# Kernel tuning notes

Measured on AMD Instinct MI355X. Metric: run time of the kernel, lower is better.

The kernel has to match this reference:

```python
import jax, jax.numpy as jnp
import numpy as np

N_NODES = 100000
N_EDGES = 1600000
NODE_DIM = 64
EDGE_DIM = 16
HIDDEN = 64
N_LAYERS = 3
N_GRAPHS = 512
BN_EPS = 1e-5


def setup_inputs() -> dict:
    key = jax.random.key(0)
    ks = jax.random.split(key, 12)
    x = jax.random.normal(ks[0], (N_NODES, NODE_DIM), dtype=jnp.float32)
    edge_index = jax.random.randint(ks[1], (2, N_EDGES), 0, N_NODES, dtype=jnp.int32)
    edge_attr = jax.random.normal(ks[2], (N_EDGES, EDGE_DIM), dtype=jnp.float32)
    batch = jnp.sort(jax.random.randint(ks[3], (N_NODES,), 0, N_GRAPHS, dtype=jnp.int32))
    s = 0.1
    # stacked per-layer params (node_dim == hidden so all layers share shapes)
    We = jax.random.normal(ks[4], (N_LAYERS, EDGE_DIM, HIDDEN), dtype=jnp.float32) * s
    be = jnp.zeros((N_LAYERS, HIDDEN), dtype=jnp.float32)
    W1 = jax.random.normal(ks[5], (N_LAYERS, HIDDEN, HIDDEN), dtype=jnp.float32) * s
    b1 = jnp.zeros((N_LAYERS, HIDDEN), dtype=jnp.float32)
    W2 = jax.random.normal(ks[6], (N_LAYERS, HIDDEN, HIDDEN), dtype=jnp.float32) * s
    b2 = jnp.zeros((N_LAYERS, HIDDEN), dtype=jnp.float32)
    gamma = jnp.ones((N_LAYERS, HIDDEN), dtype=jnp.float32)
    beta = jnp.zeros((N_LAYERS, HIDDEN), dtype=jnp.float32)
    return {"x": x, "edge_attr": edge_attr, "We": We, "be": be, "W1": W1,
            "b1": b1, "W2": W2, "b2": b2, "gamma": gamma, "beta": beta,
            "edge_index": edge_index, "batch": batch}


def reference(x, edge_attr, We, be, W1, b1, W2, b2, gamma, beta, edge_index, batch):
    src, dst = edge_index[0], edge_index[1]
    n_nodes = x.shape[0]
    z = x
    zs = []
    for l in range(We.shape[0]):
        # GINEConv: message = relu(x_j + Lin(edge_attr)); aggr = scatter_add at dst
        e = edge_attr @ We[l] + be[l]                       # [E, H]
        msg = jax.nn.relu(z[src] + e)                       # [E, H]
        aggr = jax.ops.segment_sum(msg, dst, num_segments=n_nodes)  # [N, H]
        h = z + aggr                                        # (1 + eps)*x, eps=0
        h = jax.nn.relu(h @ W1[l] + b1[l]) @ W2[l] + b2[l]  # GINE nn MLP
        h = jax.nn.relu(h)
        # BatchNorm1d in training mode: biased batch stats over nodes
        mean = jnp.mean(h, axis=0)
        var = jnp.mean(jnp.square(h - mean), axis=0)
        h = gamma[l] * (h - mean) * jax.lax.rsqrt(var + BN_EPS) + beta[l]
        z = h
        zs.append(h)
    zz = jnp.concatenate(zs, axis=1)                        # [N, L*H]
    g = jax.ops.segment_sum(zz, batch, num_segments=N_GRAPHS)  # [G, L*H]
    return zz, g
```

## Files before the change

kernel.cpp:

```cpp
#include <hip/hip_runtime.h>

#define N_NODES 100000
#define N_EDGES 1600000
#define HIDDEN 64
#define EDGE_DIM 16
#define N_LAYERS 3
#define N_GRAPHS 512
#define BN_EPS 1e-5f

#define CHUNK 2048
#define NCHUNK ((N_NODES + CHUNK - 1) / CHUNK)


__global__ void k_hist(const int* __restrict__ dst, int* __restrict__ hist) {
    int e = blockIdx.x * 256 + threadIdx.x;
    if (e < N_EDGES) atomicAdd(&hist[dst[e]], 1);
}

__global__ void k_scan_partial(const int* __restrict__ hist, int* __restrict__ partial) {
    __shared__ int sd[256];
    int c = blockIdx.x, t = threadIdx.x;
    int base = c * CHUNK + t * 8;
    int s = 0;
#pragma unroll
    for (int u = 0; u < 8; ++u) {
        int i = base + u;
        s += (i < N_NODES) ? hist[i] : 0;
    }
    sd[t] = s;
    __syncthreads();
    for (int d = 128; d > 0; d >>= 1) {
        if (t < d) sd[t] += sd[t + d];
        __syncthreads();
    }
    if (t == 0) partial[c] = sd[0];
}

__global__ void k_scan_base(const int* __restrict__ partial, int* __restrict__ cbase) {
    if (threadIdx.x == 0) {
        int r = 0;
        for (int c = 0; c < NCHUNK; ++c) { cbase[c] = r; r += partial[c]; }
    }
}

__global__ void k_scan_final(const int* __restrict__ hist, const int* __restrict__ cbase,
                             int* __restrict__ row_start, int* __restrict__ cursor) {
    __shared__ int sd[256];
    int c = blockIdx.x, t = threadIdx.x;
    int i0 = c * CHUNK + t * 8;
    int v[8];
    int s = 0;
#pragma unroll
    for (int u = 0; u < 8; ++u) {
        int i = i0 + u;
        v[u] = (i < N_NODES) ? hist[i] : 0;
        s += v[u];
    }
    sd[t] = s;
    __syncthreads();
    for (int d = 1; d < 256; d <<= 1) {
        int x = (t >= d) ? sd[t - d] : 0;
        __syncthreads();
        sd[t] += x;
        __syncthreads();
    }
    int run = cbase[c] + sd[t] - s;
#pragma unroll
    for (int u = 0; u < 8; ++u) {
        int i = i0 + u;
        if (i <= N_NODES) { row_start[i] = run; cursor[i] = run; }
        run += v[u];
    }
}

__global__ void k_fill_perm(const int* __restrict__ edge_index, int* __restrict__ cursor,
                            int* __restrict__ perm, int* __restrict__ src_sorted) {
    int e = blockIdx.x * 256 + threadIdx.x;
    if (e >= N_EDGES) return;
    int d = edge_index[N_EDGES + e];
    int p = atomicAdd(&cursor[d], 1);
    perm[p] = e;
    src_sorted[p] = edge_index[e];
}

__global__ __launch_bounds__(256) void k_gather_ea(const int* __restrict__ perm,
        const float* __restrict__ ea, float* __restrict__ ea_sorted) {
    int gid = blockIdx.x * 256 + threadIdx.x;
    if (gid >= N_EDGES * 4) return;
    int p = gid >> 2, part = gid & 3;
    int e = perm[p];
    float4 v = ((const float4*)(ea + (size_t)e * 16))[part];
    ((float4*)(ea_sorted + (size_t)p * 16))[part] = v;
}


__global__ __launch_bounds__(256) void k_aggregate(
        const float* __restrict__ z, int zstride,
        const float* __restrict__ We, const float* __restrict__ be,
        const int* __restrict__ row_start,
        const int* __restrict__ srcs, const float* __restrict__ ea,
        float* __restrict__ hin) {
    int gid = blockIdx.x * 256 + threadIdx.x;
    int node = __builtin_amdgcn_readfirstlane(gid >> 6);
    int lane = threadIdx.x & 63;
    if (node >= N_NODES) return;
    float w[16];
#pragma unroll
    for (int k = 0; k < 16; ++k) w[k] = We[k * 64 + lane];
    float bl = be[lane];
    int p0 = row_start[node], p1 = row_start[node + 1];
    float acc = 0.f;
    int p = p0;
    for (; p + 8 <= p1; p += 8) {
        int s[8];
        float zv[8], ev[8];
#pragma unroll
        for (int u = 0; u < 8; ++u) s[u] = srcs[p + u];
#pragma unroll
        for (int u = 0; u < 8; ++u) zv[u] = z[(size_t)s[u] * zstride + lane];
#pragma unroll
        for (int u = 0; u < 8; ++u) {
            const float* er = ea + (size_t)(p + u) * 16;
            float e = bl;
#pragma unroll
            for (int k = 0; k < 16; ++k) e = fmaf(er[k], w[k], e);
            ev[u] = e;
        }
#pragma unroll
        for (int u = 0; u < 8; ++u) acc += fmaxf(zv[u] + ev[u], 0.f);
    }
    for (; p + 4 <= p1; p += 4) {
        int s[4];
        float zv[4], ev[4];
#pragma unroll
        for (int u = 0; u < 4; ++u) s[u] = srcs[p + u];
#pragma unroll
        for (int u = 0; u < 4; ++u) zv[u] = z[(size_t)s[u] * zstride + lane];
#pragma unroll
        for (int u = 0; u < 4; ++u) {
            const float* er = ea + (size_t)(p + u) * 16;
            float e = bl;
#pragma unroll
            for (int k = 0; k < 16; ++k) e = fmaf(er[k], w[k], e);
            ev[u] = e;
        }
#pragma unroll
        for (int u = 0; u < 4; ++u) acc += fmaxf(zv[u] + ev[u], 0.f);
    }
    for (; p < p1; ++p) {
        int s = srcs[p];
        const float* er = ea + (size_t)p * 16;
        float zv = z[(size_t)s * zstride + lane];
        float ev = bl;
#pragma unroll
        for (int k = 0; k < 16; ++k) ev = fmaf(er[k], w[k], ev);
        acc += fmaxf(zv + ev, 0.f);
    }
    float zself = z[(size_t)node * zstride + lane];
    hin[(size_t)node * 64 + lane] = zself + acc;
}

__global__ __launch_bounds__(256) void k_mlp(
        const float* __restrict__ hin,
        const float* __restrict__ W1, const float* __restrict__ b1,
        const float* __restrict__ W2, const float* __restrict__ b2,
        float* __restrict__ hout) {
    int n = blockIdx.x * 256 + threadIdx.x;
    if (n >= N_NODES) return;
    const float4* __restrict__ hv = (const float4*)(hin + (size_t)n * 64);
    float t[64];
#pragma unroll
    for (int j = 0; j < 64; ++j) t[j] = b1[j];
    for (int kc = 0; kc < 16; ++kc) {
        float4 h4 = hv[kc];
        const float* wr = W1 + kc * 4 * 64;
#pragma unroll
        for (int j = 0; j < 64; ++j) t[j] = fmaf(h4.x, wr[j], t[j]);
#pragma unroll
        for (int j = 0; j < 64; ++j) t[j] = fmaf(h4.y, wr[64 + j], t[j]);
#pragma unroll
        for (int j = 0; j < 64; ++j) t[j] = fmaf(h4.z, wr[128 + j], t[j]);
#pragma unroll
        for (int j = 0; j < 64; ++j) t[j] = fmaf(h4.w, wr[192 + j], t[j]);
    }
#pragma unroll
    for (int j = 0; j < 64; ++j) t[j] = fmaxf(t[j], 0.f);
    float o[64];
#pragma unroll
    for (int j = 0; j < 64; ++j) o[j] = b2[j];
#pragma unroll
    for (int k = 0; k < 64; ++k) {
        const float* wr = W2 + k * 64;
        float tk = t[k];
#pragma unroll
        for (int j = 0; j < 64; ++j) o[j] = fmaf(tk, wr[j], o[j]);
    }
    float4* ov = (float4*)(hout + (size_t)n * 64);
#pragma unroll
    for (int i = 0; i < 16; ++i) {
        float4 v;
        v.x = fmaxf(o[4 * i + 0], 0.f);
        v.y = fmaxf(o[4 * i + 1], 0.f);
        v.z = fmaxf(o[4 * i + 2], 0.f);
        v.w = fmaxf(o[4 * i + 3], 0.f);
        ov[i] = v;
    }
}

__global__ __launch_bounds__(256) void k_stats(const float* __restrict__ h,
                                               float* __restrict__ ssum, float* __restrict__ ssq) {
    __shared__ float ls[64], lq[64];
    int tid = blockIdx.x * 256 + threadIdx.x;
    int nth = gridDim.x * 256;
    float4 s = {0, 0, 0, 0}, q = {0, 0, 0, 0};
    const float4* hv = (const float4*)h;
    for (int i = tid; i < N_NODES * 16; i += nth) {
        float4 v = hv[i];
        s.x += v.x; s.y += v.y; s.z += v.z; s.w += v.w;
        q.x += v.x * v.x; q.y += v.y * v.y; q.z += v.z * v.z; q.w += v.w * v.w;
    }
    if (threadIdx.x < 64) { ls[threadIdx.x] = 0.f; lq[threadIdx.x] = 0.f; }
    __syncthreads();
    int j = (threadIdx.x & 15) * 4;
    atomicAdd(&ls[j + 0], s.x); atomicAdd(&ls[j + 1], s.y);
    atomicAdd(&ls[j + 2], s.z); atomicAdd(&ls[j + 3], s.w);
    atomicAdd(&lq[j + 0], q.x); atomicAdd(&lq[j + 1], q.y);
    atomicAdd(&lq[j + 2], q.z); atomicAdd(&lq[j + 3], q.w);
    __syncthreads();
    if (threadIdx.x < 64) {
        atomicAdd(&ssum[threadIdx.x], ls[threadIdx.x]);
        atomicAdd(&ssq[threadIdx.x], lq[threadIdx.x]);
    }
}

__global__ __launch_bounds__(256) void k_norm(const float* __restrict__ h,
        const float* __restrict__ ssum, const float* __restrict__ ssq,
        const float* __restrict__ gamma, const float* __restrict__ beta,
        float* __restrict__ zzslice) {
    int i = blockIdx.x * 256 + threadIdx.x;
    if (i >= N_NODES * 16) return;
    int n = i >> 4, j4 = i & 15;
    int j = j4 * 4;
    float4 v = ((const float4*)h)[i];
    float out[4];
#pragma unroll
    for (int u = 0; u < 4; ++u) {
        float mean = ssum[j + u] * (1.f / N_NODES);
        float var = ssq[j + u] * (1.f / N_NODES) - mean * mean;
        float scale = gamma[j + u] * rsqrtf(var + BN_EPS);
        float shift = beta[j + u] - mean * scale;
        float hv = (u == 0) ? v.x : (u == 1) ? v.y : (u == 2) ? v.z : v.w;
        out[u] = fmaf(hv, scale, shift);
    }
    float4 r = {out[0], out[1], out[2], out[3]};
    *(float4*)(zzslice + (size_t)n * 192 + j4 * 4) = r;
}

#define GNODES 64
__global__ __launch_bounds__(192) void k_graph(const float* __restrict__ zz,
                                               const int* __restrict__ batch, float* __restrict__ g) {
    int j = threadIdx.x;
    int n0 = blockIdx.x * GNODES;
    int n1 = n0 + GNODES;
    if (n1 > N_NODES) n1 = N_NODES;
    if (n0 >= N_NODES) return;
    float acc = 0.f;
    int cur = batch[n0];
    for (int n = n0; n < n1; ++n) {
        int b = batch[n];
        if (b != cur) {
            atomicAdd(&g[(size_t)cur * 192 + j], acc);
            acc = 0.f;
            cur = b;
        }
        acc += zz[(size_t)n * 192 + j];
    }
    atomicAdd(&g[(size_t)cur * 192 + j], acc);
}


extern "C" void kernel_launch(void* const* d_in, const int* in_sizes, int n_in,
                              void* d_out, int out_size, void* d_ws, size_t ws_size,
                              hipStream_t stream) {
    const float* x         = (const float*)d_in[0];
    const float* edge_attr = (const float*)d_in[1];
    const float* We        = (const float*)d_in[2];
    const float* be        = (const float*)d_in[3];
    const float* W1        = (const float*)d_in[4];
    const float* b1        = (const float*)d_in[5];
    const float* W2        = (const float*)d_in[6];
    const float* b2        = (const float*)d_in[7];
    const float* gamma     = (const float*)d_in[8];
    const float* beta      = (const float*)d_in[9];
    const int* edge_index  = (const int*)d_in[10];
    const int* batch       = (const int*)d_in[11];

    float* zz = (float*)d_out;
    float* g  = zz + (size_t)N_NODES * 192;

    char* ws = (char*)d_ws;
    size_t off = 0;
    auto alloc = [&](size_t bytes) {
        void* p = ws + off;
        off = (off + bytes + 255) & ~(size_t)255;
        return p;
    };
    int* hist       = (int*)alloc((size_t)N_NODES * 4);
    int* row_start  = (int*)alloc((size_t)(N_NODES + 1) * 4);
    int* cursor     = (int*)alloc((size_t)(N_NODES + 1) * 4);
    int* partial    = (int*)alloc(64 * 4);
    int* cbase      = (int*)alloc(64 * 4);
    int* perm       = (int*)alloc((size_t)N_EDGES * 4);
    int* src_sorted = (int*)alloc((size_t)N_EDGES * 4);
    float* hin      = (float*)alloc((size_t)N_NODES * 64 * 4);
    float* hout     = (float*)alloc((size_t)N_NODES * 64 * 4);
    float* ssum     = (float*)alloc((size_t)N_LAYERS * 64 * 4);
    float* ssq      = (float*)alloc((size_t)N_LAYERS * 64 * 4);
    float* ea_sorted = (float*)alloc((size_t)N_EDGES * 16 * 4);

    hipMemsetAsync(hist, 0, (size_t)N_NODES * 4, stream);
    k_hist<<<(N_EDGES + 255) / 256, 256, 0, stream>>>(edge_index + N_EDGES, hist);
    k_scan_partial<<<NCHUNK, 256, 0, stream>>>(hist, partial);
    k_scan_base<<<1, 64, 0, stream>>>(partial, cbase);
    k_scan_final<<<NCHUNK, 256, 0, stream>>>(hist, cbase, row_start, cursor);
    k_fill_perm<<<(N_EDGES + 255) / 256, 256, 0, stream>>>(
        edge_index, cursor, perm, src_sorted);
    k_gather_ea<<<(N_EDGES * 4 + 255) / 256, 256, 0, stream>>>(
        perm, edge_attr, ea_sorted);

    hipMemsetAsync(g, 0, (size_t)N_GRAPHS * 192 * 4, stream);
    hipMemsetAsync(ssum, 0, (size_t)N_LAYERS * 64 * 4, stream);
    hipMemsetAsync(ssq, 0, (size_t)N_LAYERS * 64 * 4, stream);

    for (int l = 0; l < N_LAYERS; ++l) {
        const float* zptr = (l == 0) ? x : (zz + (size_t)(l - 1) * 64);
        int zstride = (l == 0) ? 64 : 192;
        k_aggregate<<<(N_NODES * 64 + 255) / 256, 256, 0, stream>>>(
            zptr, zstride, We + (size_t)l * EDGE_DIM * 64, be + (size_t)l * 64,
            row_start, src_sorted, ea_sorted, hin);
        k_mlp<<<(N_NODES + 255) / 256, 256, 0, stream>>>(
            hin, W1 + (size_t)l * 4096, b1 + (size_t)l * 64,
            W2 + (size_t)l * 4096, b2 + (size_t)l * 64, hout);
        k_stats<<<256, 256, 0, stream>>>(hout, ssum + l * 64, ssq + l * 64);
        k_norm<<<(N_NODES * 16 + 255) / 256, 256, 0, stream>>>(
            hout, ssum + l * 64, ssq + l * 64,
            gamma + (size_t)l * 64, beta + (size_t)l * 64, zz + (size_t)l * 64);
    }
    k_graph<<<(N_NODES + GNODES - 1) / GNODES, 192, 0, stream>>>(zz, batch, g);
}
```

Baseline: 1.074 ms.

## Store gathered node features and edge attributes in fp16 for aggregation

Edge attributes are converted to fp16 during the sort gather, and node features for the neighbor gather are kept in compact fp16 copies. These copies are x16 for layer 0 and a z16 buffer written by the norm kernel for later layers. The edge linear projection uses packed fp16 dot2 instructions with fp32 accumulation. The fill pass also writes edge id and source together as int2. The aim is to roughly halve the bytes moved in the memory-bound aggregation and edge gather, at the cost of reduced precision in messages and an extra conversion pass.

```diff
diff --git a/kernel.cpp b/kernel.cpp
--- a/kernel.cpp
+++ b/kernel.cpp
@@ -11,6 +11,9 @@
 #define CHUNK 2048
 #define NCHUNK ((N_NODES + CHUNK - 1) / CHUNK)
 
+typedef _Float16 h2 __attribute__((ext_vector_type(2)));
+typedef _Float16 h4 __attribute__((ext_vector_type(4)));
+
 
 __global__ void k_hist(const int* __restrict__ dst, int* __restrict__ hist) {
     int e = blockIdx.x * 256 + threadIdx.x;
@@ -73,40 +76,58 @@
     }
 }
 
-__global__ void k_fill_perm(const int* __restrict__ edge_index, int* __restrict__ cursor,
-                            int* __restrict__ perm, int* __restrict__ src_sorted) {
+__global__ void k_fill_es(const int* __restrict__ edge_index, int* __restrict__ cursor,
+                          int2* __restrict__ es_sorted) {
     int e = blockIdx.x * 256 + threadIdx.x;
     if (e >= N_EDGES) return;
+    int s = edge_index[e];
     int d = edge_index[N_EDGES + e];
     int p = atomicAdd(&cursor[d], 1);
-    perm[p] = e;
-    src_sorted[p] = edge_index[e];
-}
-
-__global__ __launch_bounds__(256) void k_gather_ea(const int* __restrict__ perm,
-        const float* __restrict__ ea, float* __restrict__ ea_sorted) {
+    es_sorted[p] = make_int2(e, s);
+}
+
+__global__ __launch_bounds__(256) void k_gather(const int2* __restrict__ es,
+        const float* __restrict__ ea, _Float16* __restrict__ ea16,
+        int* __restrict__ src_sorted) {
     int gid = blockIdx.x * 256 + threadIdx.x;
     if (gid >= N_EDGES * 4) return;
     int p = gid >> 2, part = gid & 3;
-    int e = perm[p];
-    float4 v = ((const float4*)(ea + (size_t)e * 16))[part];
-    ((float4*)(ea_sorted + (size_t)p * 16))[part] = v;
+    int2 r = es[p];
+    if (part == 0) src_sorted[p] = r.y;
+    float4 v = ((const float4*)(ea + (size_t)r.x * 16))[part];
+    h4 o = {(_Float16)v.x, (_Float16)v.y, (_Float16)v.z, (_Float16)v.w};
+    ((h4*)(ea16 + (size_t)p * 16))[part] = o;
+}
+
+__global__ __launch_bounds__(256) void k_cvt_x(const float* __restrict__ x,
+                                               _Float16* __restrict__ x16) {
+    int i = blockIdx.x * 256 + threadIdx.x;
+    if (i >= N_NODES * 16) return;
+    float4 v = ((const float4*)x)[i];
+    h4 o = {(_Float16)v.x, (_Float16)v.y, (_Float16)v.z, (_Float16)v.w};
+    ((h4*)x16)[i] = o;
 }
 
 
 __global__ __launch_bounds__(256) void k_aggregate(
-        const float* __restrict__ z, int zstride,
+        const float* __restrict__ zself_base, int zstride,
+        const _Float16* __restrict__ z16,
         const float* __restrict__ We, const float* __restrict__ be,
         const int* __restrict__ row_start,
-        const int* __restrict__ srcs, const float* __restrict__ ea,
+        const int* __restrict__ srcs, const _Float16* __restrict__ ea16,
         float* __restrict__ hin) {
     int gid = blockIdx.x * 256 + threadIdx.x;
     int node = __builtin_amdgcn_readfirstlane(gid >> 6);
     int lane = threadIdx.x & 63;
     if (node >= N_NODES) return;
-    float w[16];
-#pragma unroll
-    for (int k = 0; k < 16; ++k) w[k] = We[k * 64 + lane];
+    h2 w2[8];
+#pragma unroll
+    for (int i = 0; i < 8; ++i) {
+        h2 t;
+        t[0] = (_Float16)We[(2 * i) * 64 + lane];
+        t[1] = (_Float16)We[(2 * i + 1) * 64 + lane];
+        w2[i] = t;
+    }
     float bl = be[lane];
     int p0 = row_start[node], p1 = row_start[node + 1];
     float acc = 0.f;
@@ -117,13 +138,13 @@
 #pragma unroll
         for (int u = 0; u < 8; ++u) s[u] = srcs[p + u];
 #pragma unroll
-        for (int u = 0; u < 8; ++u) zv[u] = z[(size_t)s[u] * zstride + lane];
+        for (int u = 0; u < 8; ++u) zv[u] = (float)z16[(size_t)s[u] * 64 + lane];
 #pragma unroll
         for (int u = 0; u < 8; ++u) {
-            const float* er = ea + (size_t)(p + u) * 16;
+            const h2* row = (const h2*)(ea16 + (size_t)(p + u) * 16);
             float e = bl;
 #pragma unroll
-            for (int k = 0; k < 16; ++k) e = fmaf(er[k], w[k], e);
+            for (int i = 0; i < 8; ++i) e = __builtin_amdgcn_fdot2(row[i], w2[i], e, false);
             ev[u] = e;
         }
 #pragma unroll
@@ -135,13 +156,13 @@
 #pragma unroll
         for (int u = 0; u < 4; ++u) s[u] = srcs[p + u];
 #pragma unroll
-        for (int u = 0; u < 4; ++u) zv[u] = z[(size_t)s[u] * zstride + lane];
+        for (int u = 0; u < 4; ++u) zv[u] = (float)z16[(size_t)s[u] * 64 + lane];
 #pragma unroll
         for (int u = 0; u < 4; ++u) {
-            const float* er = ea + (size_t)(p + u) * 16;
+            const h2* row = (const h2*)(ea16 + (size_t)(p + u) * 16);
             float e = bl;
 #pragma unroll
-            for (int k = 0; k < 16; ++k) e = fmaf(er[k], w[k], e);
+            for (int i = 0; i < 8; ++i) e = __builtin_amdgcn_fdot2(row[i], w2[i], e, false);
             ev[u] = e;
         }
 #pragma unroll
@@ -149,14 +170,14 @@
     }
     for (; p < p1; ++p) {
         int s = srcs[p];
-        const float* er = ea + (size_t)p * 16;
-        float zv = z[(size_t)s * zstride + lane];
-        float ev = bl;
-#pragma unroll
-        for (int k = 0; k < 16; ++k) ev = fmaf(er[k], w[k], ev);
-        acc += fmaxf(zv + ev, 0.f);
-    }
-    float zself = z[(size_t)node * zstride + lane];
+        const h2* row = (const h2*)(ea16 + (size_t)p * 16);
+        float zv = (float)z16[(size_t)s * 64 + lane];
+        float e = bl;
+#pragma unroll
+        for (int i = 0; i < 8; ++i) e = __builtin_amdgcn_fdot2(row[i], w2[i], e, false);
+        acc += fmaxf(zv + e, 0.f);
+    }
+    float zself = zself_base[(size_t)node * zstride + lane];
     hin[(size_t)node * 64 + lane] = zself + acc;
 }
 
@@ -172,16 +193,16 @@
 #pragma unroll
     for (int j = 0; j < 64; ++j) t[j] = b1[j];
     for (int kc = 0; kc < 16; ++kc) {
-        float4 h4 = hv[kc];
+        float4 h4v = hv[kc];
         const float* wr = W1 + kc * 4 * 64;
 #pragma unroll
-        for (int j = 0; j < 64; ++j) t[j] = fmaf(h4.x, wr[j], t[j]);
-#pragma unroll
-        for (int j = 0; j < 64; ++j) t[j] = fmaf(h4.y, wr[64 + j], t[j]);
-#pragma unroll
-        for (int j = 0; j < 64; ++j) t[j] = fmaf(h4.z, wr[128 + j], t[j]);
-#pragma unroll
-        for (int j = 0; j < 64; ++j) t[j] = fmaf(h4.w, wr[192 + j], t[j]);
+        for (int j = 0; j < 64; ++j) t[j] = fmaf(h4v.x, wr[j], t[j]);
+#pragma unroll
+        for (int j = 0; j < 64; ++j) t[j] = fmaf(h4v.y, wr[64 + j], t[j]);
+#pragma unroll
+        for (int j = 0; j < 64; ++j) t[j] = fmaf(h4v.z, wr[128 + j], t[j]);
+#pragma unroll
+        for (int j = 0; j < 64; ++j) t[j] = fmaf(h4v.w, wr[192 + j], t[j]);
     }
 #pragma unroll
     for (int j = 0; j < 64; ++j) t[j] = fmaxf(t[j], 0.f);
@@ -236,7 +257,7 @@
 __global__ __launch_bounds__(256) void k_norm(const float* __restrict__ h,
         const float* __restrict__ ssum, const float* __restrict__ ssq,
         const float* __restrict__ gamma, const float* __restrict__ beta,
-        float* __restrict__ zzslice) {
+        float* __restrict__ zzslice, _Float16* __restrict__ z16out) {
     int i = blockIdx.x * 256 + threadIdx.x;
     if (i >= N_NODES * 16) return;
     int n = i >> 4, j4 = i & 15;
@@ -254,6 +275,10 @@
     }
     float4 r = {out[0], out[1], out[2], out[3]};
     *(float4*)(zzslice + (size_t)n * 192 + j4 * 4) = r;
+    if (z16out) {
+        h4 o = {(_Float16)out[0], (_Float16)out[1], (_Float16)out[2], (_Float16)out[3]};
+        ((h4*)(z16out + (size_t)n * 64 + j))[0] = o;
+    }
 }
 
 #define GNODES 64
@@ -305,46 +330,51 @@
         off = (off + bytes + 255) & ~(size_t)255;
         return p;
     };
-    int* hist       = (int*)alloc((size_t)N_NODES * 4);
-    int* row_start  = (int*)alloc((size_t)(N_NODES + 1) * 4);
-    int* cursor     = (int*)alloc((size_t)(N_NODES + 1) * 4);
-    int* partial    = (int*)alloc(64 * 4);
-    int* cbase      = (int*)alloc(64 * 4);
-    int* perm       = (int*)alloc((size_t)N_EDGES * 4);
-    int* src_sorted = (int*)alloc((size_t)N_EDGES * 4);
-    float* hin      = (float*)alloc((size_t)N_NODES * 64 * 4);
-    float* hout     = (float*)alloc((size_t)N_NODES * 64 * 4);
-    float* ssum     = (float*)alloc((size_t)N_LAYERS * 64 * 4);
-    float* ssq      = (float*)alloc((size_t)N_LAYERS * 64 * 4);
-    float* ea_sorted = (float*)alloc((size_t)N_EDGES * 16 * 4);
+    int* hist        = (int*)alloc((size_t)N_NODES * 4);
+    int* row_start   = (int*)alloc((size_t)(N_NODES + 1) * 4);
+    int* cursor      = (int*)alloc((size_t)(N_NODES + 1) * 4);
+    int* partial     = (int*)alloc(64 * 4);
+    int* cbase       = (int*)alloc(64 * 4);
+    int2* es_sorted  = (int2*)alloc((size_t)N_EDGES * 8);
+    int* src_sorted  = (int*)alloc((size_t)N_EDGES * 4);
+    _Float16* ea16   = (_Float16*)alloc((size_t)N_EDGES * 16 * 2);
+    _Float16* x16    = (_Float16*)alloc((size_t)N_NODES * 64 * 2);
+    _Float16* z16    = (_Float16*)alloc((size_t)N_NODES * 64 * 2);
+    float* hin       = (float*)alloc((size_t)N_NODES * 64 * 4);
+    float* hout      = (float*)alloc((size_t)N_NODES * 64 * 4);
+    float* ssum      = (float*)alloc((size_t)N_LAYERS * 64 * 4);
+    float* ssq       = (float*)alloc((size_t)N_LAYERS * 64 * 4);
 
     hipMemsetAsync(hist, 0, (size_t)N_NODES * 4, stream);
     k_hist<<<(N_EDGES + 255) / 256, 256, 0, stream>>>(edge_index + N_EDGES, hist);
     k_scan_partial<<<NCHUNK, 256, 0, stream>>>(hist, partial);
     k_scan_base<<<1, 64, 0, stream>>>(partial, cbase);
     k_scan_final<<<NCHUNK, 256, 0, stream>>>(hist, cbase, row_start, cursor);
-    k_fill_perm<<<(N_EDGES + 255) / 256, 256, 0, stream>>>(
-        edge_index, cursor, perm, src_sorted);
-    k_gather_ea<<<(N_EDGES * 4 + 255) / 256, 256, 0, stream>>>(
-        perm, edge_attr, ea_sorted);
+    k_fill_es<<<(N_EDGES + 255) / 256, 256, 0, stream>>>(edge_index, cursor, es_sorted);
+    k_gather<<<(N_EDGES * 4 + 255) / 256, 256, 0, stream>>>(
+        es_sorted, edge_attr, ea16, src_sorted);
+    k_cvt_x<<<(N_NODES * 16 + 255) / 256, 256, 0, stream>>>(x, x16);
 
     hipMemsetAsync(g, 0, (size_t)N_GRAPHS * 192 * 4, stream);
     hipMemsetAsync(ssum, 0, (size_t)N_LAYERS * 64 * 4, stream);
     hipMemsetAsync(ssq, 0, (size_t)N_LAYERS * 64 * 4, stream);
 
     for (int l = 0; l < N_LAYERS; ++l) {
-        const float* zptr = (l == 0) ? x : (zz + (size_t)(l - 1) * 64);
+        const float* zself = (l == 0) ? x : (zz + (size_t)(l - 1) * 64);
         int zstride = (l == 0) ? 64 : 192;
+        const _Float16* zsrc16 = (l == 0) ? x16 : z16;
         k_aggregate<<<(N_NODES * 64 + 255) / 256, 256, 0, stream>>>(
-            zptr, zstride, We + (size_t)l * EDGE_DIM * 64, be + (size_t)l * 64,
-            row_start, src_sorted, ea_sorted, hin);
+            zself, zstride, zsrc16,
+            We + (size_t)l * EDGE_DIM * 64, be + (size_t)l * 64,
+            row_start, src_sorted, ea16, hin);
         k_mlp<<<(N_NODES + 255) / 256, 256, 0, stream>>>(
             hin, W1 + (size_t)l * 4096, b1 + (size_t)l * 64,
             W2 + (size_t)l * 4096, b2 + (size_t)l * 64, hout);
         k_stats<<<256, 256, 0, stream>>>(hout, ssum + l * 64, ssq + l * 64);
         k_norm<<<(N_NODES * 16 + 255) / 256, 256, 0, stream>>>(
             hout, ssum + l * 64, ssq + l * 64,
-            gamma + (size_t)l * 64, beta + (size_t)l * 64, zz + (size_t)l * 64);
+            gamma + (size_t)l * 64, beta + (size_t)l * 64,
+            zz + (size_t)l * 64, (l < N_LAYERS - 1) ? z16 : (_Float16*)nullptr);
     }
     k_graph<<<(N_NODES + GNODES - 1) / GNODES, 192, 0, stream>>>(zz, batch, g);
 }
```

Measured after the change: 997.4 us. 7.1% less time.
